# Kernel tuning notes

Measured on AMD Instinct MI355X. Metric: run time of the kernel, lower is better.

## Reference

```python
import jax, jax.numpy as jnp
import numpy as np

N_NODES = 100000
BN_EPS = 1e-5


def setup_inputs() -> dict:
    key = jax.random.key(0)
    ks = jax.random.split(key, 20)
    d, h, h2, nc = 128, 128, 64, 10
    E = 1_600_000
    x = jax.random.normal(ks[0], (N_NODES, d), jnp.float32)
    ei = jax.random.randint(ks[1], (2, E), 0, N_NODES, jnp.int64)
    s = 0.05
    return {
        "x": x,
        "ei": ei,
        "W1l": jax.random.normal(ks[2], (d, h), jnp.float32) * s,
        "b1l": jax.random.normal(ks[3], (h,), jnp.float32) * s,
        "W1r": jax.random.normal(ks[4], (d, h), jnp.float32) * s,
        "g1": jax.random.uniform(ks[5], (h,), jnp.float32) + 0.5,
        "be1": jax.random.normal(ks[6], (h,), jnp.float32) * s,
        "m1": jax.random.normal(ks[7], (h,), jnp.float32) * s,
        "v1": jax.random.uniform(ks[8], (h,), jnp.float32) + 0.5,
        "W2l": jax.random.normal(ks[9], (h, h2), jnp.float32) * s,
        "b2l": jax.random.normal(ks[10], (h2,), jnp.float32) * s,
        "W2r": jax.random.normal(ks[11], (h, h2), jnp.float32) * s,
        "g2": jax.random.uniform(ks[12], (h2,), jnp.float32) + 0.5,
        "be2": jax.random.normal(ks[13], (h2,), jnp.float32) * s,
        "m2": jax.random.normal(ks[14], (h2,), jnp.float32) * s,
        "v2": jax.random.uniform(ks[15], (h2,), jnp.float32) + 0.5,
        "Wh": jax.random.normal(ks[16], (h2, nc), jnp.float32) * s,
        "bh": jax.random.normal(ks[17], (nc,), jnp.float32) * s,
    }


def _sage_conv(x, src, dst, Wl, bl, Wr):
    # PyG SAGEConv: out_i = lin_l(mean_{j->i} x_j) + lin_r(x_i)
    msg = x[src]                                              # [E, d] gather
    agg = jax.ops.segment_sum(msg, dst, num_segments=N_NODES)
    cnt = jax.ops.segment_sum(jnp.ones_like(dst, x.dtype), dst, num_segments=N_NODES)
    agg = agg / jnp.maximum(cnt, 1.0)[:, None]                # mean aggregation
    return agg @ Wl + bl + x @ Wr


def _bn(x, g, b, m, v):
    # eval-mode BatchNorm1d with running stats
    return (x - m) * (g * jax.lax.rsqrt(v + BN_EPS)) + b


def reference(x, ei, W1l, b1l, W1r, g1, be1, m1, v1,
              W2l, b2l, W2r, g2, be2, m2, v2, Wh, bh):
    src, dst = ei[0], ei[1]
    h = jax.nn.relu(_bn(_sage_conv(x, src, dst, W1l, b1l, W1r), g1, be1, m1, v1))
    # dropout p=0.1 inactive in eval mode
    h = jax.nn.relu(_bn(_sage_conv(h, src, dst, W2l, b2l, W2r), g2, be2, m2, v2))
    return h @ Wh + bh
```

## Files before the change

kernel.cpp:

```cpp
#include <hip/hip_runtime.h>
#include <hip/hip_bf16.h>
#include <stdint.h>

#define N_NODES 100000
constexpr float BN_EPS = 1e-5f;

typedef __bf16 bf16x8 __attribute__((ext_vector_type(8)));
typedef float f32x4 __attribute__((ext_vector_type(4)));

__device__ inline unsigned int pk2(float a, float b) {
    __bf16 x = (__bf16)a, y = (__bf16)b;
    return (unsigned int)__builtin_bit_cast(unsigned short, x) |
           ((unsigned int)__builtin_bit_cast(unsigned short, y) << 16);
}

__global__ __launch_bounds__(256) void k_prep(const unsigned int* __restrict__ w, int E,
                                              int* __restrict__ idx32,
                                              int* __restrict__ rank,
                                              int* __restrict__ deg, int wpB,
                                              const float* __restrict__ W1l,
                                              const float* __restrict__ W1r,
                                              const float* __restrict__ W2l,
                                              const float* __restrict__ W2r,
                                              __bf16* __restrict__ Wt1hi,
                                              __bf16* __restrict__ Wt1lo,
                                              __bf16* __restrict__ Wt2hi,
                                              __bf16* __restrict__ Wt2lo,
                                              const float* __restrict__ b1l,
                                              const float* __restrict__ g1,
                                              const float* __restrict__ be1,
                                              const float* __restrict__ m1,
                                              const float* __restrict__ v1,
                                              const float* __restrict__ b2l,
                                              const float* __restrict__ g2,
                                              const float* __restrict__ be2,
                                              const float* __restrict__ m2,
                                              const float* __restrict__ v2,
                                              float* __restrict__ bn) {
    if ((int)blockIdx.x < wpB) {
        int idx = blockIdx.x * 256 + threadIdx.x;
        const float* W; __bf16 *Whi, *Wlo; int halfN, lidx;
        if (idx < 2 * 128 * 128) {
            lidx = idx; halfN = 128; Whi = Wt1hi; Wlo = Wt1lo;
            W = ((lidx >> 7) < 128) ? W1l : W1r;
        } else {
            lidx = idx - 2 * 128 * 128;
            if (lidx >= 2 * 64 * 128) return;
            halfN = 64; Whi = Wt2hi; Wlo = Wt2lo;
            W = ((lidx >> 7) < 64) ? W2l : W2r;
        }
        int c = lidx >> 7, k = lidx & 127;
        int cc = (c < halfN) ? c : c - halfN;
        float v = W[(size_t)k * halfN + cc];
        __bf16 h = (__bf16)v;
        Whi[lidx] = h;
        Wlo[lidx] = (__bf16)(v - (float)h);
        return;
    }
    if ((int)blockIdx.x == wpB) {
        int t = threadIdx.x;
        if (t < 128) {
            float S = g1[t] * rsqrtf(v1[t] + BN_EPS);
            bn[t] = S;
            bn[128 + t] = (b1l[t] - m1[t]) * S + be1[t];
        } else if (t < 192) {
            int f = t - 128;
            float S = g2[f] * rsqrtf(v2[f] + BN_EPS);
            bn[256 + f] = S;
            bn[320 + f] = (b2l[f] - m2[f]) * S + be2[f];
        }
        return;
    }
    unsigned int wv = w[1 + 2 * (threadIdx.x & 63)];
    int f = __any(wv != 0);
    int e = (blockIdx.x - wpB - 1) * 256 + threadIdx.x;
    if (e >= E) return;
    int s = (int)(f ? w[e] : w[2 * (size_t)e]);
    int d = (int)(f ? w[E + e] : w[2 * ((size_t)E + e)]);
    idx32[e] = s;
    idx32[E + e] = d;
    rank[e] = atomicAdd(&deg[d], 1);
}

__global__ __launch_bounds__(256) void k_scan1(const int* __restrict__ deg,
                                               int* __restrict__ offs,
                                               int* __restrict__ bsum, int n) {
    __shared__ int s[256];
    int t = threadIdx.x;
    int i = blockIdx.x * 256 + t;
    int v = (i < n) ? deg[i] : 0;
    s[t] = v;
    __syncthreads();
    for (int off = 1; off < 256; off <<= 1) {
        int add = (t >= off) ? s[t - off] : 0;
        __syncthreads();
        s[t] += add;
        __syncthreads();
    }
    if (i < n) offs[i] = s[t] - v;
    if (t == 255) bsum[blockIdx.x] = s[255];
}

__global__ __launch_bounds__(256) void k_scan2(int* __restrict__ bsum, int nb) {
    __shared__ int s[256];
    __shared__ int carry;
    int t = threadIdx.x;
    if (t == 0) carry = 0;
    __syncthreads();
    for (int base = 0; base < nb; base += 256) {
        int i = base + t;
        int v = (i < nb) ? bsum[i] : 0;
        s[t] = v;
        __syncthreads();
        for (int off = 1; off < 256; off <<= 1) {
            int add = (t >= off) ? s[t - off] : 0;
            __syncthreads();
            s[t] += add;
            __syncthreads();
        }
        if (i < nb) bsum[i] = s[t] - v + carry;
        __syncthreads();
        if (t == 0) carry += s[255];
        __syncthreads();
    }
}

__global__ void k_scan3(int* __restrict__ offs, const int* __restrict__ bsum,
                        int n, int E) {
    int i = blockIdx.x * blockDim.x + threadIdx.x;
    if (i < n) offs[i] += bsum[i >> 8];
    if (i == 0) offs[n] = E;
}

template <int SPLITC>
__device__ void mfma_body(const float* __restrict__ A,
                          const __bf16* __restrict__ Wthi,
                          const __bf16* __restrict__ Wtlo,
                          __bf16* __restrict__ Cl, float* __restrict__ Cr,
                          int M, int bid) {
    constexpr int K = 128;
    __shared__ __bf16 sB[2][128][40];
    const int tid = threadIdx.x;
    const int lane = tid & 63;
    const int wave = tid >> 6;
    const int row0 = bid * 128 + wave * 32;
    const int rlo = lane & 15;
    const int rhi = lane >> 4;

    const int sc = tid >> 1;
    const int sseg = (tid & 1) * 16;

    f32x4 acc[4][2][2] = {};

    for (int k0 = 0; k0 < K; k0 += 32) {
        if (k0) __syncthreads();
        {
            const __bf16* gh = Wthi + (size_t)sc * K + k0 + sseg;
            const __bf16* gl = Wtlo + (size_t)sc * K + k0 + sseg;
            *(bf16x8*)(&sB[0][sc][sseg])     = *(const bf16x8*)gh;
            *(bf16x8*)(&sB[0][sc][sseg + 8]) = *(const bf16x8*)(gh + 8);
            *(bf16x8*)(&sB[1][sc][sseg])     = *(const bf16x8*)gl;
            *(bf16x8*)(&sB[1][sc][sseg + 8]) = *(const bf16x8*)(gl + 8);
        }
        bf16x8 ahi[2], alo[2];
        #pragma unroll
        for (int wr = 0; wr < 2; ++wr) {
            int row = row0 + wr * 16 + rlo;
            row = row < M ? row : M - 1;
            const float* ap = A + (size_t)row * K + k0 + rhi * 8;
            float4 v0 = *(const float4*)ap;
            float4 v1 = *(const float4*)(ap + 4);
            float vv[8] = {v0.x, v0.y, v0.z, v0.w, v1.x, v1.y, v1.z, v1.w};
            #pragma unroll
            for (int i = 0; i < 8; ++i) {
                __bf16 h = (__bf16)vv[i];
                ahi[wr][i] = h;
                alo[wr][i] = (__bf16)(vv[i] - (float)h);
            }
        }
        __syncthreads();
        #pragma unroll
        for (int cs = 0; cs < 4; ++cs) {
            #pragma unroll
            for (int cf = 0; cf < 2; ++cf) {
                int c = cs * 32 + cf * 16 + rlo;
                bf16x8 bhi = *(const bf16x8*)(&sB[0][c][rhi * 8]);
                bf16x8 blo = *(const bf16x8*)(&sB[1][c][rhi * 8]);
                #pragma unroll
                for (int wr = 0; wr < 2; ++wr) {
                    f32x4 a = acc[cs][wr][cf];
                    a = __builtin_amdgcn_mfma_f32_16x16x32_bf16(ahi[wr], bhi, a, 0, 0, 0);
                    a = __builtin_amdgcn_mfma_f32_16x16x32_bf16(ahi[wr], blo, a, 0, 0, 0);
                    a = __builtin_amdgcn_mfma_f32_16x16x32_bf16(alo[wr], bhi, a, 0, 0, 0);
                    acc[cs][wr][cf] = a;
                }
            }
        }
    }

    #pragma unroll
    for (int cs = 0; cs < 4; ++cs)
        #pragma unroll
        for (int cf = 0; cf < 2; ++cf) {
            int c = cs * 32 + cf * 16 + rlo;
            #pragma unroll
            for (int wr = 0; wr < 2; ++wr)
                #pragma unroll
                for (int r = 0; r < 4; ++r) {
                    int row = row0 + wr * 16 + rhi * 4 + r;
                    if (row < M) {
                        float val = acc[cs][wr][cf][r];
                        if (c < SPLITC)
                            Cl[(size_t)row * SPLITC + c] = (__bf16)val;
                        else
                            Cr[(size_t)row * (128 - SPLITC) + (c - SPLITC)] = val;
                    }
                }
        }
}

__global__ __launch_bounds__(256) void k_mfma2(const __bf16* __restrict__ A,
                                               const __bf16* __restrict__ Wthi,
                                               const __bf16* __restrict__ Wtlo,
                                               __bf16* __restrict__ Cl,
                                               float* __restrict__ Cr, int M) {
    constexpr int K = 128;
    constexpr int SPLITC = 64;
    __shared__ __bf16 sB[2][128][40];
    const int tid = threadIdx.x;
    const int lane = tid & 63;
    const int wave = tid >> 6;
    const int row0 = blockIdx.x * 128 + wave * 32;
    const int rlo = lane & 15;
    const int rhi = lane >> 4;
    const int sc = tid >> 1;
    const int sseg = (tid & 1) * 16;

    f32x4 acc[4][2][2] = {};

    for (int k0 = 0; k0 < K; k0 += 32) {
        if (k0) __syncthreads();
        {
            const __bf16* gh = Wthi + (size_t)sc * K + k0 + sseg;
            const __bf16* gl = Wtlo + (size_t)sc * K + k0 + sseg;
            *(bf16x8*)(&sB[0][sc][sseg])     = *(const bf16x8*)gh;
            *(bf16x8*)(&sB[0][sc][sseg + 8]) = *(const bf16x8*)(gh + 8);
            *(bf16x8*)(&sB[1][sc][sseg])     = *(const bf16x8*)gl;
            *(bf16x8*)(&sB[1][sc][sseg + 8]) = *(const bf16x8*)(gl + 8);
        }
        bf16x8 a[2];
        #pragma unroll
        for (int wr = 0; wr < 2; ++wr) {
            int row = row0 + wr * 16 + rlo;
            row = row < M ? row : M - 1;
            a[wr] = *(const bf16x8*)(A + (size_t)row * K + k0 + rhi * 8);
        }
        __syncthreads();
        #pragma unroll
        for (int cs = 0; cs < 4; ++cs) {
            #pragma unroll
            for (int cf = 0; cf < 2; ++cf) {
                int c = cs * 32 + cf * 16 + rlo;
                bf16x8 bhi = *(const bf16x8*)(&sB[0][c][rhi * 8]);
                bf16x8 blo = *(const bf16x8*)(&sB[1][c][rhi * 8]);
                #pragma unroll
                for (int wr = 0; wr < 2; ++wr) {
                    f32x4 v = acc[cs][wr][cf];
                    v = __builtin_amdgcn_mfma_f32_16x16x32_bf16(a[wr], bhi, v, 0, 0, 0);
                    v = __builtin_amdgcn_mfma_f32_16x16x32_bf16(a[wr], blo, v, 0, 0, 0);
                    acc[cs][wr][cf] = v;
                }
            }
        }
    }

    #pragma unroll
    for (int cs = 0; cs < 4; ++cs)
        #pragma unroll
        for (int cf = 0; cf < 2; ++cf) {
            int c = cs * 32 + cf * 16 + rlo;
            #pragma unroll
            for (int wr = 0; wr < 2; ++wr)
                #pragma unroll
                for (int r = 0; r < 4; ++r) {
                    int row = row0 + wr * 16 + rhi * 4 + r;
                    if (row < M) {
                        float val = acc[cs][wr][cf][r];
                        if (c < SPLITC)
                            Cl[(size_t)row * SPLITC + c] = (__bf16)val;
                        else
                            Cr[(size_t)row * (128 - SPLITC) + (c - SPLITC)] = val;
                    }
                }
        }
}

__global__ __launch_bounds__(256) void k_mfma_bin(const float* __restrict__ A,
                                                  const __bf16* __restrict__ Wthi,
                                                  const __bf16* __restrict__ Wtlo,
                                                  __bf16* __restrict__ Cl,
                                                  float* __restrict__ Cr, int M,
                                                  int G,
                                                  const int* __restrict__ idx32,
                                                  const int* __restrict__ rank,
                                                  const int* __restrict__ offs,
                                                  int* __restrict__ csr, int E) {
    int bid = blockIdx.x;
    if (bid < G) {
        mfma_body<128>(A, Wthi, Wtlo, Cl, nullptr, M, bid);
        return;
    }
    bid -= G;
    if (bid < G) {
        mfma_body<0>(A, Wthi + 128 * 128, Wtlo + 128 * 128, nullptr, Cr, M, bid);
        return;
    }
    bid -= G;
    int base = bid * 1024 + threadIdx.x;
    #pragma unroll
    for (int k = 0; k < 4; ++k) {
        int e = base + k * 256;
        if (e < E) {
            int d = idx32[E + e];
            csr[offs[d] + rank[e]] = idx32[e];
        }
    }
}

template <int LOGF>
__global__ __launch_bounds__(256) void k_agg(const __bf16* __restrict__ xl,
                                             const float* __restrict__ lin,
                                             const int* __restrict__ csr,
                                             const int* __restrict__ offs,
                                             const float* __restrict__ S,
                                             const float* __restrict__ T,
                                             void* __restrict__ out, int N) {
    constexpr int F = 1 << LOGF;
    constexpr int NW = (F == 128) ? 8 : 4;
    int node = blockIdx.x * 4 + (threadIdx.x >> 6);
    if (node >= N) return;
    int lane = threadIdx.x & 63;
    int sub = lane >> 4;
    int col = lane & 15;
    int beg = offs[node], end = offs[node + 1];
    float inv = 1.0f / fmaxf((float)(end - beg), 1.0f);

    float sx[NW];
    #pragma unroll
    for (int j = 0; j < NW; ++j) sx[j] = 0.f;

    int e = beg;
    while (e < end) {
        int bl = min(64, end - e);
        int myidx = (lane < bl) ? csr[e + lane] : 0;
        int u = 0;
        for (; u + 8 <= bl; u += 8) {
            int s0 = __shfl(myidx, u + sub, 64);
            int s1 = __shfl(myidx, u + 4 + sub, 64);
            if constexpr (F == 128) {
                uint4 t0 = *(const uint4*)((const char*)xl + (size_t)s0 * 256 + col * 16);
                uint4 t1 = *(const uint4*)((const char*)xl + (size_t)s1 * 256 + col * 16);
                unsigned int w0[4] = {t0.x, t0.y, t0.z, t0.w};
                unsigned int w1[4] = {t1.x, t1.y, t1.z, t1.w};
                #pragma unroll
                for (int i = 0; i < 4; ++i) {
                    sx[2 * i]     += __uint_as_float(w0[i] << 16) + __uint_as_float(w1[i] << 16);
                    sx[2 * i + 1] += __uint_as_float(w0[i] & 0xffff0000u) + __uint_as_float(w1[i] & 0xffff0000u);
                }
            } else {
                uint2 t0 = *(const uint2*)((const char*)xl + (size_t)s0 * 128 + col * 8);
                uint2 t1 = *(const uint2*)((const char*)xl + (size_t)s1 * 128 + col * 8);
                unsigned int w0[2] = {t0.x, t0.y};
                unsigned int w1[2] = {t1.x, t1.y};
                #pragma unroll
                for (int i = 0; i < 2; ++i) {
                    sx[2 * i]     += __uint_as_float(w0[i] << 16) + __uint_as_float(w1[i] << 16);
                    sx[2 * i + 1] += __uint_as_float(w0[i] & 0xffff0000u) + __uint_as_float(w1[i] & 0xffff0000u);
                }
            }
        }
        for (; u + 4 <= bl; u += 4) {
            int s0 = __shfl(myidx, u + sub, 64);
            if constexpr (F == 128) {
                uint4 t0 = *(const uint4*)((const char*)xl + (size_t)s0 * 256 + col * 16);
                unsigned int w0[4] = {t0.x, t0.y, t0.z, t0.w};
                #pragma unroll
                for (int i = 0; i < 4; ++i) {
                    sx[2 * i]     += __uint_as_float(w0[i] << 16);
                    sx[2 * i + 1] += __uint_as_float(w0[i] & 0xffff0000u);
                }
            } else {
                uint2 t0 = *(const uint2*)((const char*)xl + (size_t)s0 * 128 + col * 8);
                unsigned int w0[2] = {t0.x, t0.y};
                #pragma unroll
                for (int i = 0; i < 2; ++i) {
                    sx[2 * i]     += __uint_as_float(w0[i] << 16);
                    sx[2 * i + 1] += __uint_as_float(w0[i] & 0xffff0000u);
                }
            }
        }
        if (u < bl) {
            int rr = u + sub;
            int s0 = __shfl(myidx, rr < bl ? rr : u, 64);
            bool ok = rr < bl;
            if constexpr (F == 128) {
                uint4 t0 = *(const uint4*)((const char*)xl + (size_t)s0 * 256 + col * 16);
                unsigned int w0[4] = {t0.x, t0.y, t0.z, t0.w};
                #pragma unroll
                for (int i = 0; i < 4; ++i) {
                    sx[2 * i]     += ok ? __uint_as_float(w0[i] << 16) : 0.f;
                    sx[2 * i + 1] += ok ? __uint_as_float(w0[i] & 0xffff0000u) : 0.f;
                }
            } else {
                uint2 t0 = *(const uint2*)((const char*)xl + (size_t)s0 * 128 + col * 8);
                unsigned int w0[2] = {t0.x, t0.y};
                #pragma unroll
                for (int i = 0; i < 2; ++i) {
                    sx[2 * i]     += ok ? __uint_as_float(w0[i] << 16) : 0.f;
                    sx[2 * i + 1] += ok ? __uint_as_float(w0[i] & 0xffff0000u) : 0.f;
                }
            }
        }
        e += bl;
    }

    #pragma unroll
    for (int j = 0; j < NW; ++j) {
        sx[j] += __shfl_xor(sx[j], 16, 64);
        sx[j] += __shfl_xor(sx[j], 32, 64);
    }

    if (sub == 0) {
        if constexpr (F == 128) {
            const float4* lp = (const float4*)(lin + (size_t)node * 128 + col * 8);
            float4 l0 = lp[0], l1 = lp[1];
            const float4* Sp = (const float4*)(S + col * 8);
            const float4* Tp = (const float4*)(T + col * 8);
            float4 Sa = Sp[0], Sb = Sp[1], Ta = Tp[0], Tb = Tp[1];
            float lv[8] = {l0.x, l0.y, l0.z, l0.w, l1.x, l1.y, l1.z, l1.w};
            float Sv[8] = {Sa.x, Sa.y, Sa.z, Sa.w, Sb.x, Sb.y, Sb.z, Sb.w};
            float Tv[8] = {Ta.x, Ta.y, Ta.z, Ta.w, Tb.x, Tb.y, Tb.z, Tb.w};
            unsigned int u[4];
            #pragma unroll
            for (int i = 0; i < 4; ++i) {
                float y0 = fmaxf(fmaf(fmaf(sx[2 * i], inv, lv[2 * i]), Sv[2 * i], Tv[2 * i]), 0.f);
                float y1 = fmaxf(fmaf(fmaf(sx[2 * i + 1], inv, lv[2 * i + 1]), Sv[2 * i + 1], Tv[2 * i + 1]), 0.f);
                u[i] = pk2(y0, y1);
            }
            *(uint4*)((char*)out + (size_t)node * 256 + col * 16) = make_uint4(u[0], u[1], u[2], u[3]);
        } else {
            float4 l = *(const float4*)(lin + (size_t)node * 64 + col * 4);
            float4 Sv = *(const float4*)(S + col * 4);
            float4 Tv = *(const float4*)(T + col * 4);
            float4 o;
            o.x = fmaxf(fmaf(fmaf(sx[0], inv, l.x), Sv.x, Tv.x), 0.f);
            o.y = fmaxf(fmaf(fmaf(sx[1], inv, l.y), Sv.y, Tv.y), 0.f);
            o.z = fmaxf(fmaf(fmaf(sx[2], inv, l.z), Sv.z, Tv.z), 0.f);
            o.w = fmaxf(fmaf(fmaf(sx[3], inv, l.w), Sv.w, Tv.w), 0.f);
            *(float4*)((float*)out + (size_t)node * 64 + col * 4) = o;
        }
    }
}

__global__ __launch_bounds__(256) void k_head(const float* __restrict__ h2,
                                              const float* __restrict__ Wh,
                                              const float* __restrict__ bh,
                                              float* __restrict__ out, int M) {
    __shared__ float sW[64 * 10];
    __shared__ float sb[10];
    for (int i = threadIdx.x; i < 640; i += 256) sW[i] = Wh[i];
    if (threadIdx.x < 10) sb[threadIdx.x] = bh[threadIdx.x];
    __syncthreads();
    int n = blockIdx.x * blockDim.x + threadIdx.x;
    if (n >= M) return;
    float acc[10];
    #pragma unroll
    for (int c = 0; c < 10; ++c) acc[c] = sb[c];
    const float* hr = h2 + (size_t)n * 64;
    #pragma unroll
    for (int k = 0; k < 64; ++k) {
        float hv = hr[k];
        #pragma unroll
        for (int c = 0; c < 10; ++c) acc[c] = fmaf(hv, sW[k * 10 + c], acc[c]);
    }
    #pragma unroll
    for (int c = 0; c < 10; ++c) out[(size_t)n * 10 + c] = acc[c];
}

static inline size_t align256(size_t x) { return (x + 255) & ~(size_t)255; }

extern "C" void kernel_launch(void* const* d_in, const int* in_sizes, int n_in,
                              void* d_out, int out_size, void* d_ws, size_t ws_size,
                              hipStream_t stream) {
    const float* x   = (const float*)d_in[0];
    const void*  ei  = d_in[1];
    const float* W1l = (const float*)d_in[2];
    const float* b1l = (const float*)d_in[3];
    const float* W1r = (const float*)d_in[4];
    const float* g1  = (const float*)d_in[5];
    const float* be1 = (const float*)d_in[6];
    const float* m1  = (const float*)d_in[7];
    const float* v1  = (const float*)d_in[8];
    const float* W2l = (const float*)d_in[9];
    const float* b2l = (const float*)d_in[10];
    const float* W2r = (const float*)d_in[11];
    const float* g2  = (const float*)d_in[12];
    const float* be2 = (const float*)d_in[13];
    const float* m2  = (const float*)d_in[14];
    const float* v2  = (const float*)d_in[15];
    const float* Wh  = (const float*)d_in[16];
    const float* bh  = (const float*)d_in[17];
    float* out = (float*)d_out;

    const int N = N_NODES;
    const int E = in_sizes[1] / 2;
    const int NB = (N + 255) / 256;

    char* p = (char*)d_ws;
    int* idx32 = (int*)p;  p += align256((size_t)2 * E * 4);
    int* rank  = (int*)p;  p += align256((size_t)E * 4);
    int* csr   = (int*)p;  p += align256((size_t)E * 4);
    int* offs  = (int*)p;  p += align256((size_t)(N + 1) * 4);
    int* deg   = (int*)p;  p += align256((size_t)N * 4);
    int* bsum  = (int*)p;  p += 4096;
    float* bn  = (float*)p; p += 4096;
    __bf16* Wt1hi = (__bf16*)p; p += align256((size_t)256 * 128 * 2);
    __bf16* Wt1lo = (__bf16*)p; p += align256((size_t)256 * 128 * 2);
    __bf16* Wt2hi = (__bf16*)p; p += align256((size_t)128 * 128 * 2);
    __bf16* Wt2lo = (__bf16*)p; p += align256((size_t)128 * 128 * 2);
    __bf16* xl = (__bf16*)p; p += align256((size_t)N * 128 * 2);
    float* xr  = (float*)p;  p += (size_t)N * 128 * 4;
    __bf16* hb = (__bf16*)p; p += align256((size_t)N * 128 * 2);
    __bf16* t2l = xl;
    float* t2r  = xr;
    float* h2   = (float*)hb;

    dim3 blk(256);

    const int WPB = (2 * 128 * 128 + 2 * 64 * 128 + 255) / 256;
    int prepB = (E + 255) / 256;
    hipMemsetAsync(deg, 0, (size_t)N * 4, stream);
    k_prep<<<dim3(WPB + 1 + prepB), blk, 0, stream>>>(
        (const unsigned int*)ei, E, idx32, rank, deg, WPB,
        W1l, W1r, W2l, W2r, Wt1hi, Wt1lo, Wt2hi, Wt2lo,
        b1l, g1, be1, m1, v1, b2l, g2, be2, m2, v2, bn);

    k_scan1<<<dim3(NB), blk, 0, stream>>>(deg, offs, bsum, N);
    k_scan2<<<dim3(1), blk, 0, stream>>>(bsum, NB);
    k_scan3<<<dim3(NB), blk, 0, stream>>>(offs, bsum, N, E);

    int G = (N + 127) / 128;
    int binBlocks = (E + 1023) / 1024;
    k_mfma_bin<<<dim3(2 * G + binBlocks), blk, 0, stream>>>(
        x, Wt1hi, Wt1lo, xl, xr, N, G, idx32, rank, offs, csr, E);

    k_agg<7><<<dim3((N + 3) / 4), blk, 0, stream>>>(
        xl, xr, csr, offs, bn, bn + 128, hb, N);

    k_mfma2<<<dim3(G), blk, 0, stream>>>(hb, Wt2hi, Wt2lo, t2l, t2r, N);
    k_agg<6><<<dim3((N + 3) / 4), blk, 0, stream>>>(
        t2l, t2r, csr, offs, bn + 256, bn + 320, h2, N);

    k_head<<<dim3((N + 255) / 256), blk, 0, stream>>>(h2, Wh, bh, out, N);
}
```

Before: 288.8 us.

## Overlap edge prep with first GEMM half, pad degree counters, store root term in bf16

Splits the weight/BN prep into its own kernel. The edge conversion and degree atomics now share a launch with the W1l GEMM, and the W1r GEMM moves into the CSR scatter launch, so both latency-bound phases overlap with matrix work. Degree counters are padded to 64 bytes each to reduce atomic contention on shared cache lines. The root-term output xr is stored as bf16 instead of fp32 to halve its traffic, at some cost in precision. The padded deg array raises the memset size and makes the scan read strided memory.

```diff
diff --git a/kernel.cpp b/kernel.cpp
--- a/kernel.cpp
+++ b/kernel.cpp
@@ -14,29 +14,26 @@
            ((unsigned int)__builtin_bit_cast(unsigned short, y) << 16);
 }
 
-__global__ __launch_bounds__(256) void k_prep(const unsigned int* __restrict__ w, int E,
-                                              int* __restrict__ idx32,
-                                              int* __restrict__ rank,
-                                              int* __restrict__ deg, int wpB,
-                                              const float* __restrict__ W1l,
-                                              const float* __restrict__ W1r,
-                                              const float* __restrict__ W2l,
-                                              const float* __restrict__ W2r,
-                                              __bf16* __restrict__ Wt1hi,
-                                              __bf16* __restrict__ Wt1lo,
-                                              __bf16* __restrict__ Wt2hi,
-                                              __bf16* __restrict__ Wt2lo,
-                                              const float* __restrict__ b1l,
-                                              const float* __restrict__ g1,
-                                              const float* __restrict__ be1,
-                                              const float* __restrict__ m1,
-                                              const float* __restrict__ v1,
-                                              const float* __restrict__ b2l,
-                                              const float* __restrict__ g2,
-                                              const float* __restrict__ be2,
-                                              const float* __restrict__ m2,
-                                              const float* __restrict__ v2,
-                                              float* __restrict__ bn) {
+__global__ __launch_bounds__(256) void k_wbn(int wpB,
+                                             const float* __restrict__ W1l,
+                                             const float* __restrict__ W1r,
+                                             const float* __restrict__ W2l,
+                                             const float* __restrict__ W2r,
+                                             __bf16* __restrict__ Wt1hi,
+                                             __bf16* __restrict__ Wt1lo,
+                                             __bf16* __restrict__ Wt2hi,
+                                             __bf16* __restrict__ Wt2lo,
+                                             const float* __restrict__ b1l,
+                                             const float* __restrict__ g1,
+                                             const float* __restrict__ be1,
+                                             const float* __restrict__ m1,
+                                             const float* __restrict__ v1,
+                                             const float* __restrict__ b2l,
+                                             const float* __restrict__ g2,
+                                             const float* __restrict__ be2,
+                                             const float* __restrict__ m2,
+                                             const float* __restrict__ v2,
+                                             float* __restrict__ bn) {
     if ((int)blockIdx.x < wpB) {
         int idx = blockIdx.x * 256 + threadIdx.x;
         const float* W; __bf16 *Whi, *Wlo; int halfN, lidx;
@@ -57,79 +54,17 @@
         Wlo[lidx] = (__bf16)(v - (float)h);
         return;
     }
-    if ((int)blockIdx.x == wpB) {
-        int t = threadIdx.x;
-        if (t < 128) {
-            float S = g1[t] * rsqrtf(v1[t] + BN_EPS);
-            bn[t] = S;
-            bn[128 + t] = (b1l[t] - m1[t]) * S + be1[t];
-        } else if (t < 192) {
-            int f = t - 128;
-            float S = g2[f] * rsqrtf(v2[f] + BN_EPS);
-            bn[256 + f] = S;
-            bn[320 + f] = (b2l[f] - m2[f]) * S + be2[f];
-        }
-        return;
-    }
-    unsigned int wv = w[1 + 2 * (threadIdx.x & 63)];
-    int f = __any(wv != 0);
-    int e = (blockIdx.x - wpB - 1) * 256 + threadIdx.x;
-    if (e >= E) return;
-    int s = (int)(f ? w[e] : w[2 * (size_t)e]);
-    int d = (int)(f ? w[E + e] : w[2 * ((size_t)E + e)]);
-    idx32[e] = s;
-    idx32[E + e] = d;
-    rank[e] = atomicAdd(&deg[d], 1);
-}
-
-__global__ __launch_bounds__(256) void k_scan1(const int* __restrict__ deg,
-                                               int* __restrict__ offs,
-                                               int* __restrict__ bsum, int n) {
-    __shared__ int s[256];
     int t = threadIdx.x;
-    int i = blockIdx.x * 256 + t;
-    int v = (i < n) ? deg[i] : 0;
-    s[t] = v;
-    __syncthreads();
-    for (int off = 1; off < 256; off <<= 1) {
-        int add = (t >= off) ? s[t - off] : 0;
-        __syncthreads();
-        s[t] += add;
-        __syncthreads();
-    }
-    if (i < n) offs[i] = s[t] - v;
-    if (t == 255) bsum[blockIdx.x] = s[255];
-}
-
-__global__ __launch_bounds__(256) void k_scan2(int* __restrict__ bsum, int nb) {
-    __shared__ int s[256];
-    __shared__ int carry;
-    int t = threadIdx.x;
-    if (t == 0) carry = 0;
-    __syncthreads();
-    for (int base = 0; base < nb; base += 256) {
-        int i = base + t;
-        int v = (i < nb) ? bsum[i] : 0;
-        s[t] = v;
-        __syncthreads();
-        for (int off = 1; off < 256; off <<= 1) {
-            int add = (t >= off) ? s[t - off] : 0;
-            __syncthreads();
-            s[t] += add;
-            __syncthreads();
-        }
-        if (i < nb) bsum[i] = s[t] - v + carry;
-        __syncthreads();
-        if (t == 0) carry += s[255];
-        __syncthreads();
-    }
-}
-
-__global__ void k_scan3(int* __restrict__ offs, const int* __restrict__ bsum,
-                        int n, int E) {
-    int i = blockIdx.x * blockDim.x + threadIdx.x;
-    if (i < n) offs[i] += bsum[i >> 8];
-    if (i == 0) offs[n] = E;
+    if (t < 128) {
+        float S = g1[t] * rsqrtf(v1[t] + BN_EPS);
+        bn[t] = S;
+        bn[128 + t] = (b1l[t] - m1[t]) * S + be1[t];
+    } else if (t < 192) {
+        int f = t - 128;
+        float S = g2[f] * rsqrtf(v2[f] + BN_EPS);
+        bn[256 + f] = S;
+        bn[320 + f] = (b2l[f] - m2[f]) * S + be2[f];
+    }
 }
 
 template <int SPLITC>
@@ -217,6 +152,107 @@
                     }
                 }
         }
+}
+
+__global__ __launch_bounds__(256) void k_prep_gemm(const unsigned int* __restrict__ w,
+                                                   int E, int* __restrict__ idx32,
+                                                   int* __restrict__ rank,
+                                                   int* __restrict__ deg,
+                                                   int prepB,
+                                                   const float* __restrict__ A,
+                                                   const __bf16* __restrict__ Wthi,
+                                                   const __bf16* __restrict__ Wtlo,
+                                                   __bf16* __restrict__ Cl, int M) {
+    int bid = blockIdx.x;
+    if (bid < prepB) {
+        unsigned int wv = w[1 + 2 * (threadIdx.x & 63)];
+        int f = __any(wv != 0);
+        int e = bid * 256 + threadIdx.x;
+        if (e >= E) return;
+        int s = (int)(f ? w[e] : w[2 * (size_t)e]);
+        int d = (int)(f ? w[E + e] : w[2 * ((size_t)E + e)]);
+        idx32[e] = s;
+        idx32[E + e] = d;
+        rank[e] = atomicAdd(&deg[d << 4], 1);
+        return;
+    }
+    mfma_body<128>(A, Wthi, Wtlo, Cl, nullptr, M, bid - prepB);
+}
+
+__global__ __launch_bounds__(256) void k_scan1(const int* __restrict__ deg,
+                                               int* __restrict__ offs,
+                                               int* __restrict__ bsum, int n) {
+    __shared__ int s[256];
+    int t = threadIdx.x;
+    int i = blockIdx.x * 256 + t;
+    int v = (i < n) ? deg[i << 4] : 0;
+    s[t] = v;
+    __syncthreads();
+    for (int off = 1; off < 256; off <<= 1) {
+        int add = (t >= off) ? s[t - off] : 0;
+        __syncthreads();
+        s[t] += add;
+        __syncthreads();
+    }
+    if (i < n) offs[i] = s[t] - v;
+    if (t == 255) bsum[blockIdx.x] = s[255];
+}
+
+__global__ __launch_bounds__(256) void k_scan2(int* __restrict__ bsum, int nb) {
+    __shared__ int s[256];
+    __shared__ int carry;
+    int t = threadIdx.x;
+    if (t == 0) carry = 0;
+    __syncthreads();
+    for (int base = 0; base < nb; base += 256) {
+        int i = base + t;
+        int v = (i < nb) ? bsum[i] : 0;
+        s[t] = v;
+        __syncthreads();
+        for (int off = 1; off < 256; off <<= 1) {
+            int add = (t >= off) ? s[t - off] : 0;
+            __syncthreads();
+            s[t] += add;
+            __syncthreads();
+        }
+        if (i < nb) bsum[i] = s[t] - v + carry;
+        __syncthreads();
+        if (t == 0) carry += s[255];
+        __syncthreads();
+    }
+}
+
+__global__ void k_scan3(int* __restrict__ offs, const int* __restrict__ bsum,
+                        int n, int E) {
+    int i = blockIdx.x * blockDim.x + threadIdx.x;
+    if (i < n) offs[i] += bsum[i >> 8];
+    if (i == 0) offs[n] = E;
+}
+
+__global__ __launch_bounds__(256) void k_gemm_scat(const float* __restrict__ A,
+                                                   const __bf16* __restrict__ Wthi,
+                                                   const __bf16* __restrict__ Wtlo,
+                                                   __bf16* __restrict__ Cl, int M,
+                                                   int G,
+                                                   const int* __restrict__ idx32,
+                                                   const int* __restrict__ rank,
+                                                   const int* __restrict__ offs,
+                                                   int* __restrict__ csr, int E) {
+    int bid = blockIdx.x;
+    if (bid < G) {
+        mfma_body<128>(A, Wthi, Wtlo, Cl, nullptr, M, bid);
+        return;
+    }
+    bid -= G;
+    int base = bid * 1024 + threadIdx.x;
+    #pragma unroll
+    for (int k = 0; k < 4; ++k) {
+        int e = base + k * 256;
+        if (e < E) {
+            int d = idx32[E + e];
+            csr[offs[d] + rank[e]] = idx32[e];
+        }
+    }
 }
 
 __global__ __launch_bounds__(256) void k_mfma2(const __bf16* __restrict__ A,
@@ -295,41 +331,9 @@
         }
 }
 
-__global__ __launch_bounds__(256) void k_mfma_bin(const float* __restrict__ A,
-                                                  const __bf16* __restrict__ Wthi,
-                                                  const __bf16* __restrict__ Wtlo,
-                                                  __bf16* __restrict__ Cl,
-                                                  float* __restrict__ Cr, int M,
-                                                  int G,
-                                                  const int* __restrict__ idx32,
-                                                  const int* __restrict__ rank,
-                                                  const int* __restrict__ offs,
-                                                  int* __restrict__ csr, int E) {
-    int bid = blockIdx.x;
-    if (bid < G) {
-        mfma_body<128>(A, Wthi, Wtlo, Cl, nullptr, M, bid);
-        return;
-    }
-    bid -= G;
-    if (bid < G) {
-        mfma_body<0>(A, Wthi + 128 * 128, Wtlo + 128 * 128, nullptr, Cr, M, bid);
-        return;
-    }
-    bid -= G;
-    int base = bid * 1024 + threadIdx.x;
-    #pragma unroll
-    for (int k = 0; k < 4; ++k) {
-        int e = base + k * 256;
-        if (e < E) {
-            int d = idx32[E + e];
-            csr[offs[d] + rank[e]] = idx32[e];
-        }
-    }
-}
-
-template <int LOGF>
+template <int LOGF, bool LINBF>
 __global__ __launch_bounds__(256) void k_agg(const __bf16* __restrict__ xl,
-                                             const float* __restrict__ lin,
+                                             const void* __restrict__ lin,
                                              const int* __restrict__ csr,
                                              const int* __restrict__ offs,
                                              const float* __restrict__ S,
@@ -432,12 +436,24 @@
 
     if (sub == 0) {
         if constexpr (F == 128) {
-            const float4* lp = (const float4*)(lin + (size_t)node * 128 + col * 8);
-            float4 l0 = lp[0], l1 = lp[1];
+            float lv[8];
+            if constexpr (LINBF) {
+                uint4 l4 = *(const uint4*)((const char*)lin + ((size_t)node * 128 + col * 8) * 2);
+                unsigned int lw[4] = {l4.x, l4.y, l4.z, l4.w};
+                #pragma unroll
+                for (int i = 0; i < 4; ++i) {
+                    lv[2 * i]     = __uint_as_float(lw[i] << 16);
+                    lv[2 * i + 1] = __uint_as_float(lw[i] & 0xffff0000u);
+                }
+            } else {
+                const float4* lp = (const float4*)((const float*)lin + (size_t)node * 128 + col * 8);
+                float4 l0 = lp[0], l1 = lp[1];
+                lv[0] = l0.x; lv[1] = l0.y; lv[2] = l0.z; lv[3] = l0.w;
+                lv[4] = l1.x; lv[5] = l1.y; lv[6] = l1.z; lv[7] = l1.w;
+            }
             const float4* Sp = (const float4*)(S + col * 8);
             const float4* Tp = (const float4*)(T + col * 8);
             float4 Sa = Sp[0], Sb = Sp[1], Ta = Tp[0], Tb = Tp[1];
-            float lv[8] = {l0.x, l0.y, l0.z, l0.w, l1.x, l1.y, l1.z, l1.w};
             float Sv[8] = {Sa.x, Sa.y, Sa.z, Sa.w, Sb.x, Sb.y, Sb.z, Sb.w};
             float Tv[8] = {Ta.x, Ta.y, Ta.z, Ta.w, Tb.x, Tb.y, Tb.z, Tb.w};
             unsigned int u[4];
@@ -449,7 +465,7 @@
             }
             *(uint4*)((char*)out + (size_t)node * 256 + col * 16) = make_uint4(u[0], u[1], u[2], u[3]);
         } else {
-            float4 l = *(const float4*)(lin + (size_t)node * 64 + col * 4);
+            float4 l = *(const float4*)((const float*)lin + (size_t)node * 64 + col * 4);
             float4 Sv = *(const float4*)(S + col * 4);
             float4 Tv = *(const float4*)(T + col * 4);
             float4 o;
@@ -521,7 +537,7 @@
     int* rank  = (int*)p;  p += align256((size_t)E * 4);
     int* csr   = (int*)p;  p += align256((size_t)E * 4);
     int* offs  = (int*)p;  p += align256((size_t)(N + 1) * 4);
-    int* deg   = (int*)p;  p += align256((size_t)N * 4);
+    int* deg   = (int*)p;  p += align256((size_t)N * 64);
     int* bsum  = (int*)p;  p += 4096;
     float* bn  = (float*)p; p += 4096;
     __bf16* Wt1hi = (__bf16*)p; p += align256((size_t)256 * 128 * 2);
@@ -529,36 +545,40 @@
     __bf16* Wt2hi = (__bf16*)p; p += align256((size_t)128 * 128 * 2);
     __bf16* Wt2lo = (__bf16*)p; p += align256((size_t)128 * 128 * 2);
     __bf16* xl = (__bf16*)p; p += align256((size_t)N * 128 * 2);
-    float* xr  = (float*)p;  p += (size_t)N * 128 * 4;
+    __bf16* xr = (__bf16*)p; p += align256((size_t)N * 128 * 2);
     __bf16* hb = (__bf16*)p; p += align256((size_t)N * 128 * 2);
     __bf16* t2l = xl;
-    float* t2r  = xr;
+    float* t2r  = (float*)xr;
     float* h2   = (float*)hb;
 
     dim3 blk(256);
-
     const int WPB = (2 * 128 * 128 + 2 * 64 * 128 + 255) / 256;
     int prepB = (E + 255) / 256;
-    hipMemsetAsync(deg, 0, (size_t)N * 4, stream);
-    k_prep<<<dim3(WPB + 1 + prepB), blk, 0, stream>>>(
-        (const unsigned int*)ei, E, idx32, rank, deg, WPB,
+    int G = (N + 127) / 128;
+    int binBlocks = (E + 1023) / 1024;
+
+    hipMemsetAsync(deg, 0, (size_t)N * 64, stream);
+    k_wbn<<<dim3(WPB + 1), blk, 0, stream>>>(WPB,
         W1l, W1r, W2l, W2r, Wt1hi, Wt1lo, Wt2hi, Wt2lo,
         b1l, g1, be1, m1, v1, b2l, g2, be2, m2, v2, bn);
+
+    k_prep_gemm<<<dim3(prepB + G), blk, 0, stream>>>(
+        (const unsigned int*)ei, E, idx32, rank, deg, prepB,
+        x, Wt1hi, Wt1lo, xl, N);
 
     k_scan1<<<dim3(NB), blk, 0, stream>>>(deg, offs, bsum, N);
     k_scan2<<<dim3(1), blk, 0, stream>>>(bsum, NB);
     k_scan3<<<dim3(NB), blk, 0, stream>>>(offs, bsum, N, E);
 
-    int G = (N + 127) / 128;
-    int binBlocks = (E + 1023) / 1024;
-    k_mfma_bin<<<dim3(2 * G + binBlocks), blk, 0, stream>>>(
-        x, Wt1hi, Wt1lo, xl, xr, N, G, idx32, rank, offs, csr, E);
-
-    k_agg<7><<<dim3((N + 3) / 4), blk, 0, stream>>>(
+    k_gemm_scat<<<dim3(G + binBlocks), blk, 0, stream>>>(
+        x, Wt1hi + 128 * 128, Wt1lo + 128 * 128, xr, N, G,
+        idx32, rank, offs, csr, E);
+
+    k_agg<7, true><<<dim3((N + 3) / 4), blk, 0, stream>>>(
         xl, xr, csr, offs, bn, bn + 128, hb, N);
 
     k_mfma2<<<dim3(G), blk, 0, stream>>>(hb, Wt2hi, Wt2lo, t2l, t2r, N);
-    k_agg<6><<<dim3((N + 3) / 4), blk, 0, stream>>>(
+    k_agg<6, false><<<dim3((N + 3) / 4), blk, 0, stream>>>(
         t2l, t2r, csr, offs, bn + 256, bn + 320, h2, N);
 
     k_head<<<dim3((N + 255) / 256), blk, 0, stream>>>(h2, Wh, bh, out, N);
```

Result: slower. 302.0 us (+4.5%).

## Split layer-1 GEMM halves to overlap edge prep and CSR scatter

Applied to the files above, without the earlier changes.

Weight and BN preparation now runs in its own small kernel. The edge-index conversion and degree counting are fused with the first half of the layer-1 GEMM (the aggregated-path projection), and the second half (the root projection) is fused with the CSR scatter after the scan. Edge prep now uses a fixed 512 blocks that each loop over a chunk of edges. The aim is to fill GPU idle time by running latency-bound atomics and scatter alongside MFMA work. It adds one kernel launch and changes how the atomic contention on degree counters is spread.

```diff
diff --git a/kernel.cpp b/kernel.cpp
--- a/kernel.cpp
+++ b/kernel.cpp
@@ -14,29 +14,26 @@
            ((unsigned int)__builtin_bit_cast(unsigned short, y) << 16);
 }
 
-__global__ __launch_bounds__(256) void k_prep(const unsigned int* __restrict__ w, int E,
-                                              int* __restrict__ idx32,
-                                              int* __restrict__ rank,
-                                              int* __restrict__ deg, int wpB,
-                                              const float* __restrict__ W1l,
-                                              const float* __restrict__ W1r,
-                                              const float* __restrict__ W2l,
-                                              const float* __restrict__ W2r,
-                                              __bf16* __restrict__ Wt1hi,
-                                              __bf16* __restrict__ Wt1lo,
-                                              __bf16* __restrict__ Wt2hi,
-                                              __bf16* __restrict__ Wt2lo,
-                                              const float* __restrict__ b1l,
-                                              const float* __restrict__ g1,
-                                              const float* __restrict__ be1,
-                                              const float* __restrict__ m1,
-                                              const float* __restrict__ v1,
-                                              const float* __restrict__ b2l,
-                                              const float* __restrict__ g2,
-                                              const float* __restrict__ be2,
-                                              const float* __restrict__ m2,
-                                              const float* __restrict__ v2,
-                                              float* __restrict__ bn) {
+__global__ __launch_bounds__(256) void k_wbn(int wpB,
+                                             const float* __restrict__ W1l,
+                                             const float* __restrict__ W1r,
+                                             const float* __restrict__ W2l,
+                                             const float* __restrict__ W2r,
+                                             __bf16* __restrict__ Wt1hi,
+                                             __bf16* __restrict__ Wt1lo,
+                                             __bf16* __restrict__ Wt2hi,
+                                             __bf16* __restrict__ Wt2lo,
+                                             const float* __restrict__ b1l,
+                                             const float* __restrict__ g1,
+                                             const float* __restrict__ be1,
+                                             const float* __restrict__ m1,
+                                             const float* __restrict__ v1,
+                                             const float* __restrict__ b2l,
+                                             const float* __restrict__ g2,
+                                             const float* __restrict__ be2,
+                                             const float* __restrict__ m2,
+                                             const float* __restrict__ v2,
+                                             float* __restrict__ bn) {
     if ((int)blockIdx.x < wpB) {
         int idx = blockIdx.x * 256 + threadIdx.x;
         const float* W; __bf16 *Whi, *Wlo; int halfN, lidx;
@@ -57,79 +54,17 @@
         Wlo[lidx] = (__bf16)(v - (float)h);
         return;
     }
-    if ((int)blockIdx.x == wpB) {
-        int t = threadIdx.x;
-        if (t < 128) {
-            float S = g1[t] * rsqrtf(v1[t] + BN_EPS);
-            bn[t] = S;
-            bn[128 + t] = (b1l[t] - m1[t]) * S + be1[t];
-        } else if (t < 192) {
-            int f = t - 128;
-            float S = g2[f] * rsqrtf(v2[f] + BN_EPS);
-            bn[256 + f] = S;
-            bn[320 + f] = (b2l[f] - m2[f]) * S + be2[f];
-        }
-        return;
-    }
-    unsigned int wv = w[1 + 2 * (threadIdx.x & 63)];
-    int f = __any(wv != 0);
-    int e = (blockIdx.x - wpB - 1) * 256 + threadIdx.x;
-    if (e >= E) return;
-    int s = (int)(f ? w[e] : w[2 * (size_t)e]);
-    int d = (int)(f ? w[E + e] : w[2 * ((size_t)E + e)]);
-    idx32[e] = s;
-    idx32[E + e] = d;
-    rank[e] = atomicAdd(&deg[d], 1);
-}
-
-__global__ __launch_bounds__(256) void k_scan1(const int* __restrict__ deg,
-                                               int* __restrict__ offs,
-                                               int* __restrict__ bsum, int n) {
-    __shared__ int s[256];
     int t = threadIdx.x;
-    int i = blockIdx.x * 256 + t;
-    int v = (i < n) ? deg[i] : 0;
-    s[t] = v;
-    __syncthreads();
-    for (int off = 1; off < 256; off <<= 1) {
-        int add = (t >= off) ? s[t - off] : 0;
-        __syncthreads();
-        s[t] += add;
-        __syncthreads();
-    }
-    if (i < n) offs[i] = s[t] - v;
-    if (t == 255) bsum[blockIdx.x] = s[255];
-}
-
-__global__ __launch_bounds__(256) void k_scan2(int* __restrict__ bsum, int nb) {
-    __shared__ int s[256];
-    __shared__ int carry;
-    int t = threadIdx.x;
-    if (t == 0) carry = 0;
-    __syncthreads();
-    for (int base = 0; base < nb; base += 256) {
-        int i = base + t;
-        int v = (i < nb) ? bsum[i] : 0;
-        s[t] = v;
-        __syncthreads();
-        for (int off = 1; off < 256; off <<= 1) {
-            int add = (t >= off) ? s[t - off] : 0;
-            __syncthreads();
-            s[t] += add;
-            __syncthreads();
-        }
-        if (i < nb) bsum[i] = s[t] - v + carry;
-        __syncthreads();
-        if (t == 0) carry += s[255];
-        __syncthreads();
-    }
-}
-
-__global__ void k_scan3(int* __restrict__ offs, const int* __restrict__ bsum,
-                        int n, int E) {
-    int i = blockIdx.x * blockDim.x + threadIdx.x;
-    if (i < n) offs[i] += bsum[i >> 8];
-    if (i == 0) offs[n] = E;
+    if (t < 128) {
+        float S = g1[t] * rsqrtf(v1[t] + BN_EPS);
+        bn[t] = S;
+        bn[128 + t] = (b1l[t] - m1[t]) * S + be1[t];
+    } else if (t < 192) {
+        int f = t - 128;
+        float S = g2[f] * rsqrtf(v2[f] + BN_EPS);
+        bn[256 + f] = S;
+        bn[320 + f] = (b2l[f] - m2[f]) * S + be2[f];
+    }
 }
 
 template <int SPLITC>
@@ -217,6 +152,109 @@
                     }
                 }
         }
+}
+
+__global__ __launch_bounds__(256) void k_prep_gemm(const unsigned int* __restrict__ w,
+                                                   int E, int* __restrict__ idx32,
+                                                   int* __restrict__ rank,
+                                                   int* __restrict__ deg,
+                                                   int prepB, int chunk,
+                                                   const float* __restrict__ A,
+                                                   const __bf16* __restrict__ Wthi,
+                                                   const __bf16* __restrict__ Wtlo,
+                                                   __bf16* __restrict__ Cl, int M) {
+    int bid = blockIdx.x;
+    if (bid < prepB) {
+        unsigned int wv = w[1 + 2 * (threadIdx.x & 63)];
+        int f = __any(wv != 0);
+        int lo = bid * chunk;
+        int hi = min(lo + chunk, E);
+        for (int e = lo + (int)threadIdx.x; e < hi; e += 256) {
+            int s = (int)(f ? w[e] : w[2 * (size_t)e]);
+            int d = (int)(f ? w[E + e] : w[2 * ((size_t)E + e)]);
+            idx32[e] = s;
+            idx32[E + e] = d;
+            rank[e] = atomicAdd(&deg[d], 1);
+        }
+        return;
+    }
+    mfma_body<128>(A, Wthi, Wtlo, Cl, nullptr, M, bid - prepB);
+}
+
+__global__ __launch_bounds__(256) void k_scan1(const int* __restrict__ deg,
+                                               int* __restrict__ offs,
+                                               int* __restrict__ bsum, int n) {
+    __shared__ int s[256];
+    int t = threadIdx.x;
+    int i = blockIdx.x * 256 + t;
+    int v = (i < n) ? deg[i] : 0;
+    s[t] = v;
+    __syncthreads();
+    for (int off = 1; off < 256; off <<= 1) {
+        int add = (t >= off) ? s[t - off] : 0;
+        __syncthreads();
+        s[t] += add;
+        __syncthreads();
+    }
+    if (i < n) offs[i] = s[t] - v;
+    if (t == 255) bsum[blockIdx.x] = s[255];
+}
+
+__global__ __launch_bounds__(256) void k_scan2(int* __restrict__ bsum, int nb) {
+    __shared__ int s[256];
+    __shared__ int carry;
+    int t = threadIdx.x;
+    if (t == 0) carry = 0;
+    __syncthreads();
+    for (int base = 0; base < nb; base += 256) {
+        int i = base + t;
+        int v = (i < nb) ? bsum[i] : 0;
+        s[t] = v;
+        __syncthreads();
+        for (int off = 1; off < 256; off <<= 1) {
+            int add = (t >= off) ? s[t - off] : 0;
+            __syncthreads();
+            s[t] += add;
+            __syncthreads();
+        }
+        if (i < nb) bsum[i] = s[t] - v + carry;
+        __syncthreads();
+        if (t == 0) carry += s[255];
+        __syncthreads();
+    }
+}
+
+__global__ void k_scan3(int* __restrict__ offs, const int* __restrict__ bsum,
+                        int n, int E) {
+    int i = blockIdx.x * blockDim.x + threadIdx.x;
+    if (i < n) offs[i] += bsum[i >> 8];
+    if (i == 0) offs[n] = E;
+}
+
+__global__ __launch_bounds__(256) void k_gemm_scat(const float* __restrict__ A,
+                                                   const __bf16* __restrict__ Wthi,
+                                                   const __bf16* __restrict__ Wtlo,
+                                                   float* __restrict__ Cr, int M,
+                                                   int G,
+                                                   const int* __restrict__ idx32,
+                                                   const int* __restrict__ rank,
+                                                   const int* __restrict__ offs,
+                                                   int* __restrict__ csr, int E) {
+    int bid = blockIdx.x;
+    if (bid < G) {
+        mfma_body<0>(A, Wthi, Wtlo, nullptr, Cr, M, bid);
+        return;
+    }
+    bid -= G;
+    int base = bid * 1024 + threadIdx.x;
+    #pragma unroll
+    for (int k = 0; k < 4; ++k) {
+        int e = base + k * 256;
+        if (e < E) {
+            int d = idx32[E + e];
+            csr[offs[d] + rank[e]] = idx32[e];
+        }
+    }
 }
 
 __global__ __launch_bounds__(256) void k_mfma2(const __bf16* __restrict__ A,
@@ -293,38 +331,6 @@
                     }
                 }
         }
-}
-
-__global__ __launch_bounds__(256) void k_mfma_bin(const float* __restrict__ A,
-                                                  const __bf16* __restrict__ Wthi,
-                                                  const __bf16* __restrict__ Wtlo,
-                                                  __bf16* __restrict__ Cl,
-                                                  float* __restrict__ Cr, int M,
-                                                  int G,
-                                                  const int* __restrict__ idx32,
-                                                  const int* __restrict__ rank,
-                                                  const int* __restrict__ offs,
-                                                  int* __restrict__ csr, int E) {
-    int bid = blockIdx.x;
-    if (bid < G) {
-        mfma_body<128>(A, Wthi, Wtlo, Cl, nullptr, M, bid);
-        return;
-    }
-    bid -= G;
-    if (bid < G) {
-        mfma_body<0>(A, Wthi + 128 * 128, Wtlo + 128 * 128, nullptr, Cr, M, bid);
-        return;
-    }
-    bid -= G;
-    int base = bid * 1024 + threadIdx.x;
-    #pragma unroll
-    for (int k = 0; k < 4; ++k) {
-        int e = base + k * 256;
-        if (e < E) {
-            int d = idx32[E + e];
-            csr[offs[d] + rank[e]] = idx32[e];
-        }
-    }
 }
 
 template <int LOGF>
@@ -536,23 +542,28 @@
     float* h2   = (float*)hb;
 
     dim3 blk(256);
-
     const int WPB = (2 * 128 * 128 + 2 * 64 * 128 + 255) / 256;
-    int prepB = (E + 255) / 256;
+    int G = (N + 127) / 128;
+    int binBlocks = (E + 1023) / 1024;
+    const int prepB = 512;
+    int chunk = (E + prepB - 1) / prepB;
+
     hipMemsetAsync(deg, 0, (size_t)N * 4, stream);
-    k_prep<<<dim3(WPB + 1 + prepB), blk, 0, stream>>>(
-        (const unsigned int*)ei, E, idx32, rank, deg, WPB,
+    k_wbn<<<dim3(WPB + 1), blk, 0, stream>>>(WPB,
         W1l, W1r, W2l, W2r, Wt1hi, Wt1lo, Wt2hi, Wt2lo,
         b1l, g1, be1, m1, v1, b2l, g2, be2, m2, v2, bn);
+
+    k_prep_gemm<<<dim3(prepB + G), blk, 0, stream>>>(
+        (const unsigned int*)ei, E, idx32, rank, deg, prepB, chunk,
+        x, Wt1hi, Wt1lo, xl, N);
 
     k_scan1<<<dim3(NB), blk, 0, stream>>>(deg, offs, bsum, N);
     k_scan2<<<dim3(1), blk, 0, stream>>>(bsum, NB);
     k_scan3<<<dim3(NB), blk, 0, stream>>>(offs, bsum, N, E);
 
-    int G = (N + 127) / 128;
-    int binBlocks = (E + 1023) / 1024;
-    k_mfma_bin<<<dim3(2 * G + binBlocks), blk, 0, stream>>>(
-        x, Wt1hi, Wt1lo, xl, xr, N, G, idx32, rank, offs, csr, E);
+    k_gemm_scat<<<dim3(G + binBlocks), blk, 0, stream>>>(
+        x, Wt1hi + 128 * 128, Wt1lo + 128 * 128, xr, N, G,
+        idx32, rank, offs, csr, E);
 
     k_agg<7><<<dim3((N + 3) / 4), blk, 0, stream>>>(
         xl, xr, csr, offs, bn, bn + 128, hb, N);
```

After: 279.9 us, median of 2. 3.1% less time.
